# Kernel tuning notes

Measured on AMD Instinct MI355X. Metric: run time of the kernel, lower is better.

The kernel has to match this reference:

```python
import jax, jax.numpy as jnp
import numpy as np
import math

NUM_EMBED = 1024
EMBED_FEATS = 256
IN_FEATS = 512
COMMITMENT_COST = 0.25
B, T = 16, 4096


def setup_inputs() -> dict:
    key = jax.random.key(0)
    k1, k2, k3, k4 = jax.random.split(key, 4)
    inputs = jax.random.normal(k1, (B, IN_FEATS, T), dtype=jnp.float32)
    # Conv1d(kernel_size=1) == per-position linear: weight [E, C_in], bias [E]
    proj_w = jax.random.normal(k2, (EMBED_FEATS, IN_FEATS), dtype=jnp.float32) / np.sqrt(IN_FEATS)
    proj_b = jax.random.normal(k3, (EMBED_FEATS,), dtype=jnp.float32) * 0.01
    embed = jax.random.normal(k4, (NUM_EMBED, EMBED_FEATS), dtype=jnp.float32)
    return {"inputs": inputs, "proj_w": proj_w, "proj_b": proj_b, "embed": embed}


def reference(inputs, proj_w, proj_b, embed):
    sg = jax.lax.stop_gradient
    b, c_in, t = inputs.shape
    # 1x1 conv projection then transpose(1,-1): [B, T, E]
    x = jnp.einsum('bct,ec->bte', inputs, proj_w) + proj_b
    flat = x.reshape(-1, EMBED_FEATS)  # [B*T, E]
    d2 = (jnp.sum(flat * flat, axis=1, keepdims=True)
          + jnp.sum(embed * embed, axis=1)
          - 2.0 * flat @ embed.T)  # [B*T, num_embed]
    q_idx = jnp.argmin(d2, axis=1)  # [B*T]
    # one-hot @ embed == direct gather (same math, same gradient structure)
    z_q = embed[q_idx].reshape(x.shape)  # [B, T, E]
    vq_loss = jnp.mean((z_q - sg(x)) ** 2)
    commitment_loss = jnp.mean((sg(z_q) - x) ** 2)
    loss = vq_loss + COMMITMENT_COST * commitment_loss
    z_q_st = x + sg(z_q - x)  # straight-through
    n_tokens = flat.shape[0]
    probs = jnp.zeros((NUM_EMBED,), dtype=jnp.float32).at[q_idx].add(1.0) / n_tokens
    log_perplexity = -jnp.sum(probs * jnp.log(probs + 1e-10))
    num_spatial = n_tokens / b
    kldiv_r = math.log(NUM_EMBED) * num_spatial * jnp.ones((b, 1), dtype=jnp.float32)
    z_q_out = jnp.swapaxes(z_q_st, 1, 2)  # [B, E, T]
    return z_q_out, loss, kldiv_r, log_perplexity
```

## Files before the change

kernel.cpp:

```cpp
#include <hip/hip_runtime.h>
#include <hip/hip_bf16.h>
#include <math.h>

#define TT   4096
#define BB   16
#define NTOK 65536
#define CIN  512
#define EF   256
#define NE   1024

typedef __attribute__((ext_vector_type(8))) short bf16x8;
typedef __attribute__((ext_vector_type(4))) float f32x4;

static __device__ __forceinline__ unsigned short f2bf(float f) {
  unsigned int u = __float_as_uint(f);
  u += 0x7fffu + ((u >> 16) & 1u);
  return (unsigned short)(u >> 16);
}

#define GLL(gsrc, ldst) \
  __builtin_amdgcn_global_load_lds((const __attribute__((address_space(1))) void*)(gsrc), \
                                   (__attribute__((address_space(3))) void*)(ldst), 16, 0, 0)

__global__ __launch_bounds__(256) void k_prep(const float* __restrict__ Wf,
                                              const float* __restrict__ Ef,
                                              unsigned short* __restrict__ Wbf,
                                              unsigned short* __restrict__ Ebf,
                                              float* __restrict__ e_norm) {
  int bid = blockIdx.x;
  if (bid < 512) {
    int i = bid * 256 + threadIdx.x;
    Wbf[i] = f2bf(Wf[i]);
  } else if (bid < 1536) {
    int i = (bid - 512) * 256 + threadIdx.x;
    Ebf[i] = f2bf(-2.0f * Ef[i]);
  } else {
    int w = threadIdx.x >> 6, l = threadIdx.x & 63;
    int k = (bid - 1536) * 4 + w;
    const float4 v4 = ((const float4*)(Ef + (size_t)k * EF))[l];
    float s = v4.x * v4.x + v4.y * v4.y + v4.z * v4.z + v4.w * v4.w;
    for (int off = 32; off; off >>= 1) s += __shfl_down(s, off);
    if (l == 0) e_norm[k] = s;
  }
}

__global__ __launch_bounds__(512, 2) void k_fused(const float* __restrict__ in,
                                                  const unsigned short* __restrict__ Wbf,
                                                  const float* __restrict__ bias,
                                                  const unsigned short* __restrict__ Ebf,
                                                  const float* __restrict__ e_norm,
                                                  const float* __restrict__ embed,
                                                  unsigned int* __restrict__ hist,
                                                  float* __restrict__ sse,
                                                  float* __restrict__ out) {
  __shared__ unsigned short lds[32768];
  unsigned short* as_ = lds;
  unsigned short* bs  = lds + 8192;
  unsigned short* xs  = lds;

  int tid = threadIdx.x;
  int w = tid >> 6, l = tid & 63;
  int l15 = l & 15, quad = l >> 4;
  int tq = w & 1, eq = w >> 1;
  int cg = w & 3, th = w >> 2;
  int tok0 = blockIdx.x * 128;
  const float* src = in + (size_t)(tok0 >> 12) * CIN * TT + (tok0 & 4095);

  f32x4 acc[4][4];
#pragma unroll
  for (int a = 0; a < 4; ++a)
#pragma unroll
    for (int b = 0; b < 4; ++b) acc[a][b] = (f32x4){0.f, 0.f, 0.f, 0.f};

  float v[16];
  {
    const float* s0 = src + (size_t)(cg * 16) * TT + th * 64 + l;
#pragma unroll
    for (int i = 0; i < 16; ++i) v[i] = s0[(size_t)i * TT];
  }
  for (int ks = 0; ks < 8; ++ks) {
    int k0 = ks * 64;
#pragma unroll
    for (int i = 0; i < 4; ++i) {
      int g = i * 512 + tid;
      int row = g >> 3, pc = g & 7, lc = pc ^ (row & 7);
      GLL(Wbf + (size_t)row * CIN + k0 + lc * 8, bs + g * 8);
    }
    __builtin_amdgcn_sched_barrier(0);
    int trow = th * 64 + l;
#pragma unroll
    for (int cc = 0; cc < 2; ++cc) {
      alignas(16) unsigned short tmp[8];
#pragma unroll
      for (int j = 0; j < 8; ++j) tmp[j] = f2bf(v[cc * 8 + j]);
      int c8 = cg * 2 + cc;
      int pc2 = c8 ^ (trow & 7);
      *(bf16x8*)(as_ + trow * 64 + pc2 * 8) = *(const bf16x8*)tmp;
    }
    if (ks < 7) {
      const float* s0 = src + (size_t)(k0 + 64 + cg * 16) * TT + th * 64 + l;
#pragma unroll
      for (int i = 0; i < 16; ++i) v[i] = s0[(size_t)i * TT];
      __builtin_amdgcn_sched_barrier(0);
      asm volatile("s_waitcnt vmcnt(16) lgkmcnt(0)\n\ts_barrier" ::: "memory");
    } else {
      asm volatile("s_waitcnt vmcnt(0) lgkmcnt(0)\n\ts_barrier" ::: "memory");
    }
#pragma unroll
    for (int kstep = 0; kstep < 2; ++kstep) {
      int ck = kstep * 4 + quad;
      bf16x8 af[4], bfr[4];
#pragma unroll
      for (int msub = 0; msub < 4; ++msub) {
        int row = tq * 64 + msub * 16 + l15;
        int pa = ck ^ (row & 7);
        af[msub] = *(const bf16x8*)(as_ + row * 64 + pa * 8);
      }
#pragma unroll
      for (int nsub = 0; nsub < 4; ++nsub) {
        int row = eq * 64 + nsub * 16 + l15;
        int pb = ck ^ (row & 7);
        bfr[nsub] = *(const bf16x8*)(bs + row * 64 + pb * 8);
      }
      __builtin_amdgcn_s_setprio(1);
#pragma unroll
      for (int msub = 0; msub < 4; ++msub)
#pragma unroll
        for (int nsub = 0; nsub < 4; ++nsub)
          acc[msub][nsub] = __builtin_amdgcn_mfma_f32_16x16x32_bf16(af[msub], bfr[nsub],
                                                                    acc[msub][nsub], 0, 0, 0);
      __builtin_amdgcn_s_setprio(0);
    }
    asm volatile("s_waitcnt lgkmcnt(0)\n\ts_barrier" ::: "memory");
  }

  float xsq = 0.f;
#pragma unroll
  for (int nsub = 0; nsub < 4; ++nsub) {
    int e = eq * 64 + nsub * 16 + l15;
    float bv = bias[e];
    int cx = e >> 3;
#pragma unroll
    for (int msub = 0; msub < 4; ++msub)
#pragma unroll
      for (int reg = 0; reg < 4; ++reg) {
        int m = tq * 64 + msub * 16 + quad * 4 + reg;
        float x = acc[msub][nsub][reg] + bv;
        xsq += x * x;
        int pcx = cx ^ (m & 31);
        xs[m * 256 + pcx * 8 + (e & 7)] = f2bf(x);
      }
  }
  __syncthreads();

  int g3 = w & 3, h = w >> 2;
  bf16x8 af[2][8];
#pragma unroll
  for (int msub = 0; msub < 2; ++msub)
#pragma unroll
    for (int kst = 0; kst < 8; ++kst) {
      int row = g3 * 32 + msub * 16 + l15;
      int c32 = kst * 4 + quad;
      int pcx = c32 ^ (row & 31);
      af[msub][kst] = *(const bf16x8*)(xs + row * 256 + pcx * 8);
    }
  __syncthreads();

  float* entab = (float*)(lds + 24576);
  {
    float2 ev = *(const float2*)(e_norm + (tid << 1));
    *(float2*)(entab + (tid << 1)) = ev;
  }
  __builtin_amdgcn_sched_barrier(0);
#pragma unroll
  for (int i = 0; i < 2; ++i) {
    int g = i * 512 + tid;
    int row = g >> 5, pcc = g & 31, lc = pcc ^ row;
    GLL(Ebf + (size_t)row * EF + lc * 8, lds + g * 8);
  }
  __builtin_amdgcn_sched_barrier(0);

  float best_v[2][4];
  int best_i[2][4];
#pragma unroll
  for (int a = 0; a < 2; ++a)
#pragma unroll
    for (int b = 0; b < 4; ++b) { best_v[a][b] = 3.0e38f; best_i[a][b] = 0; }

  int r3 = h * 16 + l15;
  unsigned short* eb = lds;
  unsigned short* pf = lds + 8192;
  int c0 = 0;
#pragma unroll 1
  for (int chunk = 0; chunk < 32; ++chunk, c0 += 32) {
    if (chunk < 31) {
#pragma unroll
      for (int i = 0; i < 2; ++i) {
        int g = i * 512 + tid;
        int row = g >> 5, pcc = g & 31, lc = pcc ^ row;
        GLL(Ebf + (size_t)(c0 + 32 + row) * EF + lc * 8, pf + g * 8);
      }
      __builtin_amdgcn_sched_barrier(0);
      asm volatile("s_waitcnt vmcnt(2) lgkmcnt(0)\n\ts_barrier" ::: "memory");
    } else {
      asm volatile("s_waitcnt vmcnt(0) lgkmcnt(0)\n\ts_barrier" ::: "memory");
    }
    float en = entab[c0 + r3];
    f32x4 dacc[2];
    dacc[0] = (f32x4){en, en, en, en};
    dacc[1] = (f32x4){en, en, en, en};
    __builtin_amdgcn_s_setprio(1);
#pragma unroll
    for (int kst = 0; kst < 8; ++kst) {
      int cc = kst * 4 + quad;
      int pc = cc ^ r3;
      bf16x8 bfr = *(const bf16x8*)(eb + r3 * 256 + pc * 8);
      dacc[0] = __builtin_amdgcn_mfma_f32_16x16x32_bf16(af[0][kst], bfr, dacc[0], 0, 0, 0);
      dacc[1] = __builtin_amdgcn_mfma_f32_16x16x32_bf16(af[1][kst], bfr, dacc[1], 0, 0, 0);
    }
    __builtin_amdgcn_s_setprio(0);
    int code = c0 + r3;
#pragma unroll
    for (int msub = 0; msub < 2; ++msub)
#pragma unroll
      for (int reg = 0; reg < 4; ++reg) {
        float vv = dacc[msub][reg];
        if (vv < best_v[msub][reg]) { best_v[msub][reg] = vv; best_i[msub][reg] = code; }
      }
    eb = pf;
    pf += 8192;
    if (pf == lds + 24576) pf = lds;
  }

#pragma unroll
  for (int msub = 0; msub < 2; ++msub)
#pragma unroll
    for (int reg = 0; reg < 4; ++reg) {
      float vv = best_v[msub][reg];
      int idx = best_i[msub][reg];
#pragma unroll
      for (int off = 8; off; off >>= 1) {
        float ov = __shfl_xor(vv, off, 16);
        int oi = __shfl_xor(idx, off, 16);
        if (ov < vv || (ov == vv && oi < idx)) { vv = ov; idx = oi; }
      }
      best_v[msub][reg] = vv;
      best_i[msub][reg] = idx;
    }
  float* red_v = (float*)lds;
  int* red_i = (int*)lds + 256;
  float* xred = (float*)lds + 512;
  float* svred = (float*)lds + 520;
  int* fidx_w = (int*)lds + 544;
  if (l15 == 0) {
#pragma unroll
    for (int msub = 0; msub < 2; ++msub)
#pragma unroll
      for (int reg = 0; reg < 4; ++reg) {
        int tokloc = g3 * 32 + msub * 16 + quad * 4 + reg;
        red_v[h * 128 + tokloc] = best_v[msub][reg];
        red_i[h * 128 + tokloc] = best_i[msub][reg];
      }
  }
  for (int off = 32; off; off >>= 1) xsq += __shfl_down(xsq, off);
  if (l == 0) xred[w] = xsq;
  __syncthreads();
  if (tid < 128) {
    float v0 = red_v[tid], v1 = red_v[128 + tid];
    int i0 = red_i[tid], i1 = red_i[128 + tid];
    float vv; int idx;
    if (v1 < v0 || (v1 == v0 && i1 < i0)) { vv = v1; idx = i1; } else { vv = v0; idx = i0; }
    fidx_w[tid] = idx;
    atomicAdd(&hist[idx], 1u);
    for (int off = 32; off; off >>= 1) vv += __shfl_down(vv, off);
    if ((tid & 63) == 0) svred[tid >> 6] = vv;
  }
  __syncthreads();
  if (tid == 0) {
    float tot = svred[0] + svred[1];
#pragma unroll
    for (int i = 0; i < 8; ++i) tot += xred[i];
    atomicAdd(sse, tot);
  }

  const int* fidx = (const int*)lds + 544;
  float* zq = (float*)lds + 1024;
  int bnum = tok0 >> 12, t0 = tok0 & 4095;
  float* outb = out + (((size_t)bnum * EF) << 12) + t0;
#pragma unroll 1
  for (int et = 0; et < 4; ++et) {
    int e0 = et * 64;
#pragma unroll
    for (int rr = 0; rr < 4; ++rr) {
      int tl = rr * 32 + (tid >> 4);
      const float4 g4 = *(const float4*)(embed + (size_t)fidx[tl] * EF + e0 + (tid & 15) * 4);
      float* zr = zq + tl * 65 + (tid & 15) * 4;
      zr[0] = g4.x; zr[1] = g4.y; zr[2] = g4.z; zr[3] = g4.w;
    }
    __syncthreads();
#pragma unroll
    for (int rr = 0; rr < 4; ++rr) {
      int e = rr * 16 + (tid >> 5);
      int tc = (tid & 31) * 4;
      float4 o4;
      o4.x = zq[(tc + 0) * 65 + e];
      o4.y = zq[(tc + 1) * 65 + e];
      o4.z = zq[(tc + 2) * 65 + e];
      o4.w = zq[(tc + 3) * 65 + e];
      *(float4*)(outb + ((size_t)(e0 + e) << 12) + tc) = o4;
    }
    if (et < 3) __syncthreads();
  }
}

__global__ __launch_bounds__(256) void k_final(const unsigned int* __restrict__ hist,
                                               const float* __restrict__ sse,
                                               float* __restrict__ out) {
  __shared__ float red[4];
  int tid = threadIdx.x;
  float local = 0.f;
  for (int i = tid; i < NE; i += 256) {
    float p = (float)hist[i] * (1.0f / 65536.0f);
    local -= p * logf(p + 1e-10f);
  }
  for (int off = 32; off; off >>= 1) local += __shfl_down(local, off);
  if ((tid & 63) == 0) red[tid >> 6] = local;
  __syncthreads();
  if (tid == 0) {
    float lp = red[0] + red[1] + red[2] + red[3];
    out[16777216] = 1.25f * sse[0] / 16777216.0f;
    out[16777233] = lp;
  }
  if (tid < 16) out[16777217 + tid] = 6.93147180559945f * 4096.0f;
}

extern "C" void kernel_launch(void* const* d_in, const int* in_sizes, int n_in,
                              void* d_out, int out_size, void* d_ws, size_t ws_size,
                              hipStream_t stream) {
  const float* inputs = (const float*)d_in[0];
  const float* proj_w = (const float*)d_in[1];
  const float* proj_b = (const float*)d_in[2];
  const float* embed = (const float*)d_in[3];
  float* out = (float*)d_out;
  char* ws = (char*)d_ws;

  unsigned short* Wbf  = (unsigned short*)(ws);
  unsigned short* Ebf  = (unsigned short*)(ws + 262144);
  float* e_norm        = (float*)(ws + 786432);
  unsigned int* hist   = (unsigned int*)(ws + 1052672);
  float* sse           = (float*)(ws + 1056768);
  if (ws_size < 1056772) return;

  hipMemsetAsync(ws + 1052672, 0, 4100, stream);

  k_prep<<<1792, 256, 0, stream>>>(proj_w, embed, Wbf, Ebf, e_norm);
  k_fused<<<512, 512, 0, stream>>>(inputs, Wbf, proj_b, Ebf, e_norm, embed, hist, sse, out);
  k_final<<<1, 256, 0, stream>>>(hist, sse, out);
}
```

Measured before the change: 293.1 us.

## Read weights and codebook directly from global instead of LDS staging

Drops the async global-to-LDS staging of the projection weights and codebook. MFMA B fragments are now loaded straight from global/L2 into registers, and the input tile is double-buffered in LDS with plain __syncthreads. It also adds nontemporal loads for the input and nontemporal scalar stores for the output. This removes LDS traffic and the hand-written waitcnt/barrier pipelining, but every wave now issues uncoalesced-ish global loads for shared data with no prefetch overlap. Output stores become scalar rather than float4.

```diff
diff --git a/kernel.cpp b/kernel.cpp
--- a/kernel.cpp
+++ b/kernel.cpp
@@ -17,10 +17,6 @@
   u += 0x7fffu + ((u >> 16) & 1u);
   return (unsigned short)(u >> 16);
 }
-
-#define GLL(gsrc, ldst) \
-  __builtin_amdgcn_global_load_lds((const __attribute__((address_space(1))) void*)(gsrc), \
-                                   (__attribute__((address_space(3))) void*)(ldst), 16, 0, 0)
 
 __global__ __launch_bounds__(256) void k_prep(const float* __restrict__ Wf,
                                               const float* __restrict__ Ef,
@@ -54,9 +50,7 @@
                                                   float* __restrict__ sse,
                                                   float* __restrict__ out) {
   __shared__ unsigned short lds[32768];
-  unsigned short* as_ = lds;
-  unsigned short* bs  = lds + 8192;
-  unsigned short* xs  = lds;
+  unsigned short* xs = lds;
 
   int tid = threadIdx.x;
   int w = tid >> 6, l = tid & 63;
@@ -76,17 +70,11 @@
   {
     const float* s0 = src + (size_t)(cg * 16) * TT + th * 64 + l;
 #pragma unroll
-    for (int i = 0; i < 16; ++i) v[i] = s0[(size_t)i * TT];
+    for (int i = 0; i < 16; ++i) v[i] = __builtin_nontemporal_load(&s0[(size_t)i * TT]);
   }
   for (int ks = 0; ks < 8; ++ks) {
     int k0 = ks * 64;
-#pragma unroll
-    for (int i = 0; i < 4; ++i) {
-      int g = i * 512 + tid;
-      int row = g >> 3, pc = g & 7, lc = pc ^ (row & 7);
-      GLL(Wbf + (size_t)row * CIN + k0 + lc * 8, bs + g * 8);
-    }
-    __builtin_amdgcn_sched_barrier(0);
+    unsigned short* aw = lds + (ks & 1) * 8192;
     int trow = th * 64 + l;
 #pragma unroll
     for (int cc = 0; cc < 2; ++cc) {
@@ -95,44 +83,40 @@
       for (int j = 0; j < 8; ++j) tmp[j] = f2bf(v[cc * 8 + j]);
       int c8 = cg * 2 + cc;
       int pc2 = c8 ^ (trow & 7);
-      *(bf16x8*)(as_ + trow * 64 + pc2 * 8) = *(const bf16x8*)tmp;
+      *(bf16x8*)(aw + trow * 64 + pc2 * 8) = *(const bf16x8*)tmp;
     }
     if (ks < 7) {
       const float* s0 = src + (size_t)(k0 + 64 + cg * 16) * TT + th * 64 + l;
 #pragma unroll
-      for (int i = 0; i < 16; ++i) v[i] = s0[(size_t)i * TT];
-      __builtin_amdgcn_sched_barrier(0);
-      asm volatile("s_waitcnt vmcnt(16) lgkmcnt(0)\n\ts_barrier" ::: "memory");
-    } else {
-      asm volatile("s_waitcnt vmcnt(0) lgkmcnt(0)\n\ts_barrier" ::: "memory");
-    }
+      for (int i = 0; i < 16; ++i) v[i] = __builtin_nontemporal_load(&s0[(size_t)i * TT]);
+    }
+    __syncthreads();
 #pragma unroll
     for (int kstep = 0; kstep < 2; ++kstep) {
       int ck = kstep * 4 + quad;
-      bf16x8 af[4], bfr[4];
+      bf16x8 af4[4], bfr[4];
 #pragma unroll
       for (int msub = 0; msub < 4; ++msub) {
         int row = tq * 64 + msub * 16 + l15;
         int pa = ck ^ (row & 7);
-        af[msub] = *(const bf16x8*)(as_ + row * 64 + pa * 8);
+        af4[msub] = *(const bf16x8*)(aw + row * 64 + pa * 8);
       }
 #pragma unroll
       for (int nsub = 0; nsub < 4; ++nsub) {
-        int row = eq * 64 + nsub * 16 + l15;
-        int pb = ck ^ (row & 7);
-        bfr[nsub] = *(const bf16x8*)(bs + row * 64 + pb * 8);
+        int erow = eq * 64 + nsub * 16 + l15;
+        bfr[nsub] = *(const bf16x8*)(Wbf + (size_t)erow * CIN + k0 + ck * 8);
       }
       __builtin_amdgcn_s_setprio(1);
 #pragma unroll
       for (int msub = 0; msub < 4; ++msub)
 #pragma unroll
         for (int nsub = 0; nsub < 4; ++nsub)
-          acc[msub][nsub] = __builtin_amdgcn_mfma_f32_16x16x32_bf16(af[msub], bfr[nsub],
+          acc[msub][nsub] = __builtin_amdgcn_mfma_f32_16x16x32_bf16(af4[msub], bfr[nsub],
                                                                     acc[msub][nsub], 0, 0, 0);
       __builtin_amdgcn_s_setprio(0);
     }
-    asm volatile("s_waitcnt lgkmcnt(0)\n\ts_barrier" ::: "memory");
-  }
+  }
+  __syncthreads();
 
   float xsq = 0.f;
 #pragma unroll
@@ -166,20 +150,6 @@
     }
   __syncthreads();
 
-  float* entab = (float*)(lds + 24576);
-  {
-    float2 ev = *(const float2*)(e_norm + (tid << 1));
-    *(float2*)(entab + (tid << 1)) = ev;
-  }
-  __builtin_amdgcn_sched_barrier(0);
-#pragma unroll
-  for (int i = 0; i < 2; ++i) {
-    int g = i * 512 + tid;
-    int row = g >> 5, pcc = g & 31, lc = pcc ^ row;
-    GLL(Ebf + (size_t)row * EF + lc * 8, lds + g * 8);
-  }
-  __builtin_amdgcn_sched_barrier(0);
-
   float best_v[2][4];
   int best_i[2][4];
 #pragma unroll
@@ -188,35 +158,24 @@
     for (int b = 0; b < 4; ++b) { best_v[a][b] = 3.0e38f; best_i[a][b] = 0; }
 
   int r3 = h * 16 + l15;
-  unsigned short* eb = lds;
-  unsigned short* pf = lds + 8192;
-  int c0 = 0;
+  const unsigned short* ebase = Ebf + (size_t)r3 * EF + quad * 8;
 #pragma unroll 1
-  for (int chunk = 0; chunk < 32; ++chunk, c0 += 32) {
-    if (chunk < 31) {
-#pragma unroll
-      for (int i = 0; i < 2; ++i) {
-        int g = i * 512 + tid;
-        int row = g >> 5, pcc = g & 31, lc = pcc ^ row;
-        GLL(Ebf + (size_t)(c0 + 32 + row) * EF + lc * 8, pf + g * 8);
-      }
-      __builtin_amdgcn_sched_barrier(0);
-      asm volatile("s_waitcnt vmcnt(2) lgkmcnt(0)\n\ts_barrier" ::: "memory");
-    } else {
-      asm volatile("s_waitcnt vmcnt(0) lgkmcnt(0)\n\ts_barrier" ::: "memory");
-    }
-    float en = entab[c0 + r3];
+  for (int chunk = 0; chunk < 32; ++chunk) {
+    int c0 = chunk * 32;
+    const unsigned short* ep = ebase + (size_t)c0 * EF;
+    float en = e_norm[c0 + r3];
+    bf16x8 bfr[8];
+#pragma unroll
+    for (int kst = 0; kst < 8; ++kst)
+      bfr[kst] = *(const bf16x8*)(ep + kst * 32);
     f32x4 dacc[2];
     dacc[0] = (f32x4){en, en, en, en};
-    dacc[1] = (f32x4){en, en, en, en};
+    dacc[1] = dacc[0];
     __builtin_amdgcn_s_setprio(1);
 #pragma unroll
     for (int kst = 0; kst < 8; ++kst) {
-      int cc = kst * 4 + quad;
-      int pc = cc ^ r3;
-      bf16x8 bfr = *(const bf16x8*)(eb + r3 * 256 + pc * 8);
-      dacc[0] = __builtin_amdgcn_mfma_f32_16x16x32_bf16(af[0][kst], bfr, dacc[0], 0, 0, 0);
-      dacc[1] = __builtin_amdgcn_mfma_f32_16x16x32_bf16(af[1][kst], bfr, dacc[1], 0, 0, 0);
+      dacc[0] = __builtin_amdgcn_mfma_f32_16x16x32_bf16(af[0][kst], bfr[kst], dacc[0], 0, 0, 0);
+      dacc[1] = __builtin_amdgcn_mfma_f32_16x16x32_bf16(af[1][kst], bfr[kst], dacc[1], 0, 0, 0);
     }
     __builtin_amdgcn_s_setprio(0);
     int code = c0 + r3;
@@ -227,9 +186,6 @@
         float vv = dacc[msub][reg];
         if (vv < best_v[msub][reg]) { best_v[msub][reg] = vv; best_i[msub][reg] = code; }
       }
-    eb = pf;
-    pf += 8192;
-    if (pf == lds + 24576) pf = lds;
   }
 
 #pragma unroll
@@ -301,13 +257,12 @@
 #pragma unroll
     for (int rr = 0; rr < 4; ++rr) {
       int e = rr * 16 + (tid >> 5);
-      int tc = (tid & 31) * 4;
-      float4 o4;
-      o4.x = zq[(tc + 0) * 65 + e];
-      o4.y = zq[(tc + 1) * 65 + e];
-      o4.z = zq[(tc + 2) * 65 + e];
-      o4.w = zq[(tc + 3) * 65 + e];
-      *(float4*)(outb + ((size_t)(e0 + e) << 12) + tc) = o4;
+      float* orow = outb + ((size_t)(e0 + e) << 12);
+#pragma unroll
+      for (int j = 0; j < 4; ++j) {
+        int t = (tid & 31) + 32 * j;
+        __builtin_nontemporal_store(zq[t * 65 + e], &orow[t]);
+      }
     }
     if (et < 3) __syncthreads();
   }
```

Result: slower. 380.4 us (+29.8%).

## Deepen prefetch pipelines in projection and codebook search, use nontemporal loads/stores

Applied to the files above, without the earlier changes.

The projection GEMM now double-buffers the weight tile in LDS and holds two register sets of input activations, so loads are issued two k-steps ahead. The codebook search moves from a 3-slot to a 4-slot LDS ring with three chunks in flight, and adds an explicit barrier at the end of each chunk. Input loads and output stores become nontemporal, and the output store changes from float4 to scalar coalesced writes. LDS per block grows and register pressure rises, which may cut occupancy at 2 blocks per CU.

```diff
diff --git a/kernel.cpp b/kernel.cpp
--- a/kernel.cpp
+++ b/kernel.cpp
@@ -53,10 +53,9 @@
                                                   unsigned int* __restrict__ hist,
                                                   float* __restrict__ sse,
                                                   float* __restrict__ out) {
-  __shared__ unsigned short lds[32768];
-  unsigned short* as_ = lds;
-  unsigned short* bs  = lds + 8192;
-  unsigned short* xs  = lds;
+  __shared__ unsigned short lds[36864];
+  unsigned short* abuf = lds;
+  unsigned short* xs = lds;
 
   int tid = threadIdx.x;
   int w = tid >> 6, l = tid & 63;
@@ -72,62 +71,80 @@
 #pragma unroll
     for (int b = 0; b < 4; ++b) acc[a][b] = (f32x4){0.f, 0.f, 0.f, 0.f};
 
-  float v[16];
+  float v0[16], v1[16];
   {
-    const float* s0 = src + (size_t)(cg * 16) * TT + th * 64 + l;
-#pragma unroll
-    for (int i = 0; i < 16; ++i) v[i] = s0[(size_t)i * TT];
-  }
-  for (int ks = 0; ks < 8; ++ks) {
-    int k0 = ks * 64;
+    const float* sA = src + (size_t)(cg * 16) * TT + th * 64 + l;
+#pragma unroll
+    for (int i = 0; i < 16; ++i) v0[i] = __builtin_nontemporal_load(&sA[(size_t)i * TT]);
+    __builtin_amdgcn_sched_barrier(0);
 #pragma unroll
     for (int i = 0; i < 4; ++i) {
       int g = i * 512 + tid;
       int row = g >> 3, pc = g & 7, lc = pc ^ (row & 7);
-      GLL(Wbf + (size_t)row * CIN + k0 + lc * 8, bs + g * 8);
-    }
-    __builtin_amdgcn_sched_barrier(0);
-    int trow = th * 64 + l;
+      GLL(Wbf + (size_t)row * CIN + lc * 8, lds + 4096 + g * 8);
+    }
+    __builtin_amdgcn_sched_barrier(0);
+    const float* sB = src + (size_t)(64 + cg * 16) * TT + th * 64 + l;
+#pragma unroll
+    for (int i = 0; i < 16; ++i) v1[i] = __builtin_nontemporal_load(&sB[(size_t)i * TT]);
+    __builtin_amdgcn_sched_barrier(0);
+  }
+  int trow = th * 64 + l;
+#pragma unroll
+  for (int ks = 0; ks < 8; ++ks) {
+    unsigned short* wb = lds + 4096 + (ks & 1) * 16384;
+    const float* vc = (ks & 1) ? v1 : v0;
 #pragma unroll
     for (int cc = 0; cc < 2; ++cc) {
       alignas(16) unsigned short tmp[8];
 #pragma unroll
-      for (int j = 0; j < 8; ++j) tmp[j] = f2bf(v[cc * 8 + j]);
+      for (int j = 0; j < 8; ++j) tmp[j] = f2bf(vc[cc * 8 + j]);
       int c8 = cg * 2 + cc;
       int pc2 = c8 ^ (trow & 7);
-      *(bf16x8*)(as_ + trow * 64 + pc2 * 8) = *(const bf16x8*)tmp;
+      *(bf16x8*)(abuf + trow * 64 + pc2 * 8) = *(const bf16x8*)tmp;
     }
     if (ks < 7) {
-      const float* s0 = src + (size_t)(k0 + 64 + cg * 16) * TT + th * 64 + l;
-#pragma unroll
-      for (int i = 0; i < 16; ++i) v[i] = s0[(size_t)i * TT];
-      __builtin_amdgcn_sched_barrier(0);
-      asm volatile("s_waitcnt vmcnt(16) lgkmcnt(0)\n\ts_barrier" ::: "memory");
-    } else {
-      asm volatile("s_waitcnt vmcnt(0) lgkmcnt(0)\n\ts_barrier" ::: "memory");
-    }
+#pragma unroll
+      for (int i = 0; i < 4; ++i) {
+        int g = i * 512 + tid;
+        int row = g >> 3, pc = g & 7, lc = pc ^ (row & 7);
+        GLL(Wbf + (size_t)row * CIN + (ks + 1) * 64 + lc * 8,
+            lds + 4096 + ((ks + 1) & 1) * 16384 + g * 8);
+      }
+    }
+    __builtin_amdgcn_sched_barrier(0);
+    if (ks < 6) {
+      float* vn = (ks & 1) ? v1 : v0;
+      const float* sN = src + (size_t)((ks + 2) * 64 + cg * 16) * TT + th * 64 + l;
+#pragma unroll
+      for (int i = 0; i < 16; ++i) vn[i] = __builtin_nontemporal_load(&sN[(size_t)i * TT]);
+    }
+    __builtin_amdgcn_sched_barrier(0);
+    if (ks < 6)       asm volatile("s_waitcnt vmcnt(36) lgkmcnt(0)\n\ts_barrier" ::: "memory");
+    else if (ks == 6) asm volatile("s_waitcnt vmcnt(20) lgkmcnt(0)\n\ts_barrier" ::: "memory");
+    else              asm volatile("s_waitcnt vmcnt(0) lgkmcnt(0)\n\ts_barrier" ::: "memory");
 #pragma unroll
     for (int kstep = 0; kstep < 2; ++kstep) {
       int ck = kstep * 4 + quad;
-      bf16x8 af[4], bfr[4];
+      bf16x8 af4[4], bfr[4];
 #pragma unroll
       for (int msub = 0; msub < 4; ++msub) {
         int row = tq * 64 + msub * 16 + l15;
         int pa = ck ^ (row & 7);
-        af[msub] = *(const bf16x8*)(as_ + row * 64 + pa * 8);
+        af4[msub] = *(const bf16x8*)(abuf + row * 64 + pa * 8);
       }
 #pragma unroll
       for (int nsub = 0; nsub < 4; ++nsub) {
         int row = eq * 64 + nsub * 16 + l15;
         int pb = ck ^ (row & 7);
-        bfr[nsub] = *(const bf16x8*)(bs + row * 64 + pb * 8);
+        bfr[nsub] = *(const bf16x8*)(wb + row * 64 + pb * 8);
       }
       __builtin_amdgcn_s_setprio(1);
 #pragma unroll
       for (int msub = 0; msub < 4; ++msub)
 #pragma unroll
         for (int nsub = 0; nsub < 4; ++nsub)
-          acc[msub][nsub] = __builtin_amdgcn_mfma_f32_16x16x32_bf16(af[msub], bfr[nsub],
+          acc[msub][nsub] = __builtin_amdgcn_mfma_f32_16x16x32_bf16(af4[msub], bfr[nsub],
                                                                     acc[msub][nsub], 0, 0, 0);
       __builtin_amdgcn_s_setprio(0);
     }
@@ -166,18 +183,20 @@
     }
   __syncthreads();
 
-  float* entab = (float*)(lds + 24576);
+  float* entab = (float*)(lds + 32768);
   {
     float2 ev = *(const float2*)(e_norm + (tid << 1));
     *(float2*)(entab + (tid << 1)) = ev;
   }
   __builtin_amdgcn_sched_barrier(0);
 #pragma unroll
-  for (int i = 0; i < 2; ++i) {
-    int g = i * 512 + tid;
-    int row = g >> 5, pcc = g & 31, lc = pcc ^ row;
-    GLL(Ebf + (size_t)row * EF + lc * 8, lds + g * 8);
-  }
+  for (int c = 0; c < 3; ++c)
+#pragma unroll
+    for (int i = 0; i < 2; ++i) {
+      int g = i * 512 + tid;
+      int row = g >> 5, pcc = g & 31, lc = pcc ^ row;
+      GLL(Ebf + (size_t)(c * 32 + row) * EF + lc * 8, lds + c * 8192 + g * 8);
+    }
   __builtin_amdgcn_sched_barrier(0);
 
   float best_v[2][4];
@@ -188,27 +207,27 @@
     for (int b = 0; b < 4; ++b) { best_v[a][b] = 3.0e38f; best_i[a][b] = 0; }
 
   int r3 = h * 16 + l15;
-  unsigned short* eb = lds;
-  unsigned short* pf = lds + 8192;
-  int c0 = 0;
 #pragma unroll 1
-  for (int chunk = 0; chunk < 32; ++chunk, c0 += 32) {
-    if (chunk < 31) {
+  for (int chunk = 0; chunk < 32; ++chunk) {
+    unsigned short* eb = lds + (chunk & 3) * 8192;
+    int c0 = chunk * 32;
+    if (chunk < 29) {
+      unsigned short* ebn = lds + ((chunk + 3) & 3) * 8192;
 #pragma unroll
       for (int i = 0; i < 2; ++i) {
         int g = i * 512 + tid;
         int row = g >> 5, pcc = g & 31, lc = pcc ^ row;
-        GLL(Ebf + (size_t)(c0 + 32 + row) * EF + lc * 8, pf + g * 8);
+        GLL(Ebf + (size_t)(c0 + 96 + row) * EF + lc * 8, ebn + g * 8);
       }
       __builtin_amdgcn_sched_barrier(0);
-      asm volatile("s_waitcnt vmcnt(2) lgkmcnt(0)\n\ts_barrier" ::: "memory");
+      asm volatile("s_waitcnt vmcnt(6) lgkmcnt(0)\n\ts_barrier" ::: "memory");
     } else {
       asm volatile("s_waitcnt vmcnt(0) lgkmcnt(0)\n\ts_barrier" ::: "memory");
     }
     float en = entab[c0 + r3];
     f32x4 dacc[2];
     dacc[0] = (f32x4){en, en, en, en};
-    dacc[1] = (f32x4){en, en, en, en};
+    dacc[1] = dacc[0];
     __builtin_amdgcn_s_setprio(1);
 #pragma unroll
     for (int kst = 0; kst < 8; ++kst) {
@@ -227,9 +246,7 @@
         float vv = dacc[msub][reg];
         if (vv < best_v[msub][reg]) { best_v[msub][reg] = vv; best_i[msub][reg] = code; }
       }
-    eb = pf;
-    pf += 8192;
-    if (pf == lds + 24576) pf = lds;
+    asm volatile("s_waitcnt lgkmcnt(0)\n\ts_barrier" ::: "memory");
   }
 
 #pragma unroll
@@ -266,10 +283,10 @@
   if (l == 0) xred[w] = xsq;
   __syncthreads();
   if (tid < 128) {
-    float v0 = red_v[tid], v1 = red_v[128 + tid];
+    float v0r = red_v[tid], v1r = red_v[128 + tid];
     int i0 = red_i[tid], i1 = red_i[128 + tid];
     float vv; int idx;
-    if (v1 < v0 || (v1 == v0 && i1 < i0)) { vv = v1; idx = i1; } else { vv = v0; idx = i0; }
+    if (v1r < v0r || (v1r == v0r && i1 < i0)) { vv = v1r; idx = i1; } else { vv = v0r; idx = i0; }
     fidx_w[tid] = idx;
     atomicAdd(&hist[idx], 1u);
     for (int off = 32; off; off >>= 1) vv += __shfl_down(vv, off);
@@ -301,13 +318,12 @@
 #pragma unroll
     for (int rr = 0; rr < 4; ++rr) {
       int e = rr * 16 + (tid >> 5);
-      int tc = (tid & 31) * 4;
-      float4 o4;
-      o4.x = zq[(tc + 0) * 65 + e];
-      o4.y = zq[(tc + 1) * 65 + e];
-      o4.z = zq[(tc + 2) * 65 + e];
-      o4.w = zq[(tc + 3) * 65 + e];
-      *(float4*)(outb + ((size_t)(e0 + e) << 12) + tc) = o4;
+      float* orow = outb + ((size_t)(e0 + e) << 12);
+#pragma unroll
+      for (int j = 0; j < 4; ++j) {
+        int t = (tid & 31) + 32 * j;
+        __builtin_nontemporal_store(zq[t * 65 + e], &orow[t]);
+      }
     }
     if (et < 3) __syncthreads();
   }
```

Measured after the change: 293.5 us. No clear change (+0.1%).
